# Optimization experiments

Measured on AMD Instinct MI355X. Metric: run time of the kernel, lower is better.

## Reference

```python
import jax, jax.numpy as jnp
import numpy as np
import math

B, H, L = 8, 512, 2048
CH = 1          # channels
D2 = 32         # d_state // 2 (conjugate pairs)
DT_MIN, DT_MAX = 0.001, 0.1


def setup_inputs() -> dict:
    key = jax.random.key(0)
    ks = jax.random.split(key, 7)
    u = jax.random.normal(ks[0], (B, H, L), dtype=jnp.float32)
    # Chebyshev initialization (SimpleS4)
    h_scale = jnp.exp(jnp.arange(H, dtype=jnp.float32) / H * math.log(DT_MAX / DT_MIN))
    angles = jnp.arange(D2, dtype=jnp.float32) * jnp.pi
    theta = jnp.broadcast_to(angles[None, None, :], (CH, H, D2)).astype(jnp.float32) + 0.0
    a = -(jnp.broadcast_to(h_scale[None, :, None], (CH, H, D2)).astype(jnp.float32) + 0.0)
    b = jax.random.normal(ks[1], (CH, H, D2), dtype=jnp.float32)
    c = jax.random.normal(ks[2], (CH, H, D2), dtype=jnp.float32)
    x0 = jax.random.normal(ks[3], (CH, H, D2), dtype=jnp.float32)
    D = jax.random.normal(ks[4], (CH, H), dtype=jnp.float32)
    lim = 1.0 / math.sqrt(CH * H)
    W = jax.random.uniform(ks[5], (H, CH * H), minval=-lim, maxval=lim, dtype=jnp.float32)
    bias = jax.random.uniform(ks[6], (H,), minval=-lim, maxval=lim, dtype=jnp.float32)
    return dict(u=u, a=a, theta=theta, b=b, c=c, x0=x0, D=D, W=W, bias=bias)


def fft_conv(u, f):
    # u: (B,H,L), f: (C,H,L) -> causal conv (B,C,H,L) via zero-padded FFT
    n = 2 * u.shape[-1]
    u_f = jnp.fft.rfft(u, n=n)
    f_f = jnp.fft.rfft(f, n=n)
    y = jnp.fft.irfft(jnp.einsum('bhl,chl->bchl', u_f, f_f), n=n)
    return y[..., : u.shape[-1]]


def s4_forward(u, a, theta, b, c, x0, D, W, bias):
    Bsz, Hd, l = u.shape
    T = 1.0 / (l - 1)                                   # quadrature step
    z = T * jnp.arange(l, dtype=u.dtype)                # (L,)
    aa = -jnp.abs(a)                                    # (C,H,D2) stable decay
    # Vandermonde-like basis: exp(a z) cos(theta z), shape (C,H,D2,L)
    base = jnp.exp(aa[..., None] * z) * jnp.cos(theta[..., None] * z)
    q = b * c                                           # (C,H,D2)
    f = 2.0 * T * jnp.einsum('chd,chdl->chl', q, base)  # SSM kernel (C,H,L)
    y = fft_conv(u, f)                                  # (B,C,H,L)
    # trapezoid-rule endpoint correction
    y = y - 0.5 * (jnp.einsum('ch,bhl->bchl', f[:, :, 0], u)
                   + jnp.einsum('chl,bh->bchl', f, u[:, :, 0]))
    # initial-state contribution (x0 term)
    k0 = 2.0 * jnp.einsum('chd,chdl->chl', c * x0, base)
    y = y + k0[None]
    # skip connection D*u
    y = y + jnp.einsum('ch,bhl->bchl', D, u)
    y = y.reshape(Bsz, CH * Hd, l)                      # (B, C*H, L)
    # NonLinear head: GELU -> pointwise Linear(C*H -> H) (transposed conv1x1)
    y = jax.nn.gelu(y, approximate=False)
    out = jnp.einsum('hf,bfl->bhl', W, y) + bias[None, :, None]
    return out


def reference(u, a, theta, b, c, x0, D, W, bias):
    return s4_forward(u, a, theta, b, c, x0, D, W, bias)
```

## Files before the change

### kernel.cpp

```cpp
#include <hip/hip_runtime.h>
#include <hip/hip_bf16.h>

#define B_  8
#define H_  512
#define L_  2048
#define D2_ 32
#define NC_ 64
#define LC_ 32
#define EP  36

typedef __attribute__((ext_vector_type(8))) short short8;
typedef __attribute__((ext_vector_type(8))) _Float16 half8;
typedef __attribute__((ext_vector_type(2))) _Float16 half2v;
typedef __attribute__((ext_vector_type(4))) float float4v;

__device__ __forceinline__ half2v pk_fma16(half2v a, half2v b, half2v c) {
    return __builtin_elementwise_fma(a, b, c);
}

__device__ __forceinline__ float gelu_fast(float x) {
    float q = x * fmaf(0.044715f, x * x, 1.0f);
    float s = __expf(-1.5957691216057308f * q);
    return __fdividef(x, 1.0f + s);
}

__device__ __forceinline__ unsigned pack_bf16x2(float x, float y) {
    __hip_bfloat162 p = __float22bfloat162_rn(make_float2(x, y));
    return *(unsigned*)&p;
}
__device__ __forceinline__ float2 unpack_bf16x2(unsigned v) {
    __hip_bfloat162 p = *(__hip_bfloat162*)&v;
    return __bfloat1622float2(p);
}
__device__ __forceinline__ unsigned pack_f16x2(float x, float y) {
    auto v = __builtin_amdgcn_cvt_pkrtz(x, y);
    return *(unsigned*)&v;
}

__device__ __forceinline__ void load_lds16(const void* g, void* l) {
    __builtin_amdgcn_global_load_lds((const __attribute__((address_space(1))) unsigned int*)g,
                                     (__attribute__((address_space(3))) unsigned int*)l, 16, 0, 0);
}

__global__ __launch_bounds__(256) void fkprep_kernel(
        const float* __restrict__ a, const float* __restrict__ th,
        const float* __restrict__ bb, const float* __restrict__ cc,
        const float* __restrict__ x0, const float* __restrict__ W,
        __hip_bfloat16* __restrict__ Wb, unsigned* __restrict__ FKf,
        _Float16* __restrict__ AB, _Float16* __restrict__ CB,
        _Float16* __restrict__ WPh) {
    __shared__ float avs[32], tvs[32], qds[32], gxs[32], f_lds[32];
    int h = blockIdx.x;
    int t = threadIdx.x;
    const float T = 1.0f / (float)(L_ - 1);
    Wb[(size_t)h * 512 + t]       = __float2bfloat16(W[(size_t)h * 512 + t]);
    Wb[(size_t)h * 512 + t + 256] = __float2bfloat16(W[(size_t)h * 512 + t + 256]);
    if (t < 32) {
        int d = t;
        float av = -fabsf(a[h * D2_ + d]);
        float tv = th[h * D2_ + d];
        avs[d] = av; tvs[d] = tv;
        qds[d] = bb[h * D2_ + d] * cc[h * D2_ + d];
        gxs[d] = 2.0f * cc[h * D2_ + d] * x0[h * D2_ + d];
        #pragma unroll
        for (int k = 0; k < 6; ++k) {
            float len = (float)(32 << k);
            float e2  = __expf(av * T * len);
            float an  = tv * T * len;
            WPh[((size_t)h * 6 + k) * 64 + d]      = (_Float16)(e2 * __cosf(an));
            WPh[((size_t)h * 6 + k) * 64 + 32 + d] = (_Float16)(e2 * __sinf(an));
        }
    }
    __syncthreads();
    int q4 = t & 3, lc = t >> 2;
    float z0 = T * (float)(lc * 32);
    float pr[8], pi[8], wr[8], wi[8], qd[8], gx[8];
    #pragma unroll
    for (int j = 0; j < 8; ++j) {
        int d = q4 * 8 + j;
        float aa = avs[d], tv = tvs[d];
        float e0 = __expf(aa * z0);
        pr[j] = e0 * __cosf(tv * z0);
        pi[j] = e0 * __sinf(tv * z0);
        float e1 = __expf(aa * T);
        wr[j] = e1 * __cosf(tv * T);
        wi[j] = e1 * __sinf(tv * T);
        qd[j] = qds[d];
        gx[j] = gxs[d];
    }
    for (int i = 0; i < 32; ++i) {
        float fa = 0.f, ka = 0.f;
        #pragma unroll
        for (int j = 0; j < 8; ++j) {
            fa = fmaf(qd[j], pr[j], fa);
            ka = fmaf(gx[j], pr[j], ka);
            float nr = fmaf(pr[j], wr[j], -(pi[j] * wi[j]));
            float ni = fmaf(pr[j], wi[j],  (pi[j] * wr[j]));
            pr[j] = nr; pi[j] = ni;
        }
        fa += __shfl_xor(fa, 1); fa += __shfl_xor(fa, 2);
        ka += __shfl_xor(ka, 1); ka += __shfl_xor(ka, 2);
        if (q4 == 0) {
            float fv = 2.0f * T * fa;
            FKf[(size_t)h * L_ + lc * 32 + i] = pack_bf16x2(fv, ka);
            if (lc == 0) f_lds[i] = fv;
        }
    }
    __syncthreads();
    for (int e = t; e < 64 * 32; e += 256) {
        int m = e >> 5, i = e & 31;
        int d = m & 31;
        float av = avs[d], tv = tvs[d];
        float z  = T * (float)(31 - i);
        float ex = __expf(av * z);
        float v  = (m < 32) ? ex * __cosf(tv * z) : ex * __sinf(tv * z);
        AB[(size_t)h * 2048 + e] = (_Float16)v;
    }
    for (int e = t; e < 32 * 96; e += 256) {
        int i = e / 96, k = e - i * 96;
        float v = 0.f;
        if (k < 32) {
            if (k <= i) v = f_lds[i - k];
        } else {
            int d = (k < 64) ? k - 32 : k - 64;
            float av = avs[d], tv = tvs[d];
            float qs = 2.0f * T * qds[d];
            float z  = T * (float)(i + 1);
            float ex = __expf(av * z);
            v = (k < 64) ? qs * ex * __cosf(tv * z) : -qs * ex * __sinf(tv * z);
        }
        CB[(size_t)h * 3072 + e] = (_Float16)v;
    }
}

__global__ __launch_bounds__(128, 6) void scan_mfma_kernel(
        const float* __restrict__ u, const _Float16* __restrict__ AB,
        const _Float16* __restrict__ CB, const unsigned* __restrict__ WPh,
        const float* __restrict__ Dp, const unsigned* __restrict__ FKf,
        __hip_bfloat16* __restrict__ y) {
    __shared__ __align__(16) unsigned El[64 * EP];
    int wid = threadIdx.x >> 6, lane = threadIdx.x & 63;
    int h = blockIdx.x, b = blockIdx.y;
    int ln = lane & 15, qq = lane >> 4;
    const float* ug = u + (size_t)(b * H_ + h) * L_;

    half8 uf[4];
    #pragma unroll
    for (int nb = 0; nb < 4; ++nb) {
        const float* p = ug + (nb * 16 + ln) * 32 + qq * 8;
        float4 a0 = *(const float4*)p;
        float4 a1 = *(const float4*)(p + 4);
        unsigned* vp = (unsigned*)&uf[nb];
        vp[0] = pack_f16x2(a0.x, a0.y);
        vp[1] = pack_f16x2(a0.z, a0.w);
        vp[2] = pack_f16x2(a1.x, a1.y);
        vp[3] = pack_f16x2(a1.z, a1.w);
    }

    const _Float16* ABh = AB + (size_t)h * 2048;
    int j0 = wid * 8 + qq * 2;
    #pragma unroll
    for (int e = 0; e < 2; ++e) {
        half8 af = *(const half8*)&ABh[(e * 32 + wid * 16 + ln) * 32 + qq * 8];
        #pragma unroll
        for (int nb = 0; nb < 4; ++nb) {
            float4v acc = (float4v){0.f, 0.f, 0.f, 0.f};
            acc = __builtin_amdgcn_mfma_f32_16x16x32_f16(af, uf[nb], acc, 0, 0, 0);
            unsigned p0 = pack_f16x2(acc[0], acc[1]);
            unsigned p1 = pack_f16x2(acc[2], acc[3]);
            *(uint2*)&El[(nb * 16 + ln) * EP + e * 16 + j0] = make_uint2(p0, p1);
        }
    }
    asm volatile("s_waitcnt lgkmcnt(0)" ::: "memory");
    __builtin_amdgcn_sched_barrier(0);

    int c = lane;
    unsigned sr[8], si[8];
    {
        const unsigned* rp = &El[c * EP + wid * 8];
        uint4 r0 = *(const uint4*)rp;
        uint4 r1 = *(const uint4*)(rp + 4);
        uint4 i0 = *(const uint4*)(rp + 16);
        uint4 i1 = *(const uint4*)(rp + 20);
        sr[0]=r0.x; sr[1]=r0.y; sr[2]=r0.z; sr[3]=r0.w;
        sr[4]=r1.x; sr[5]=r1.y; sr[6]=r1.z; sr[7]=r1.w;
        si[0]=i0.x; si[1]=i0.y; si[2]=i0.z; si[3]=i0.w;
        si[4]=i1.x; si[5]=i1.y; si[6]=i1.z; si[7]=i1.w;
    }
    const unsigned* mpb = WPh + (size_t)h * 6 * 32;
    #pragma unroll
    for (int st = 0; st < 6; ++st) {
        int off = 1 << st;
        int src = (c - off) & 63;
        bool act = c >= off;
        const unsigned* mp = mpb + st * 32 + wid * 8;
        #pragma unroll
        for (int jj = 0; jj < 8; ++jj) {
            unsigned prp = (unsigned)__shfl((int)sr[jj], src);
            unsigned pip = (unsigned)__shfl((int)si[jj], src);
            if (!act) { prp = 0u; pip = 0u; }
            unsigned mru = mp[jj];
            unsigned miu = mp[16 + jj];
            unsigned min_ = miu ^ 0x80008000u;
            half2v pr = *(half2v*)&prp, pi = *(half2v*)&pip;
            half2v Mr = *(half2v*)&mru, Mi = *(half2v*)&miu, Mni = *(half2v*)&min_;
            half2v s_r = *(half2v*)&sr[jj], s_i = *(half2v*)&si[jj];
            half2v nr = pk_fma16(pr, Mr, pk_fma16(pi, Mni, s_r));
            half2v ni = pk_fma16(pr, Mi, pk_fma16(pi, Mr,  s_i));
            sr[jj] = *(unsigned*)&nr; si[jj] = *(unsigned*)&ni;
        }
    }
    {
        int srcm1 = (c - 1) & 63;
        #pragma unroll
        for (int jj = 0; jj < 8; ++jj) {
            unsigned a0 = (unsigned)__shfl((int)sr[jj], srcm1);
            unsigned b0 = (unsigned)__shfl((int)si[jj], srcm1);
            if (c == 0) { a0 = 0u; b0 = 0u; }
            sr[jj] = a0; si[jj] = b0;
        }
    }
    {
        unsigned* wp = &El[c * EP + wid * 8];
        *(uint4*)wp        = make_uint4(sr[0], sr[1], sr[2], sr[3]);
        *(uint4*)(wp + 4)  = make_uint4(sr[4], sr[5], sr[6], sr[7]);
        *(uint4*)(wp + 16) = make_uint4(si[0], si[1], si[2], si[3]);
        *(uint4*)(wp + 20) = make_uint4(si[4], si[5], si[6], si[7]);
    }
    const unsigned* fgh = FKf + (size_t)h * L_;
    uint4 fkp[2][2];
    #pragma unroll
    for (int nbi = 0; nbi < 2; ++nbi) {
        int col = (2 * wid + nbi) * 16 + ln;
        fkp[nbi][0] = *(const uint4*)&fgh[col * 32 + qq * 4];
        fkp[nbi][1] = *(const uint4*)&fgh[col * 32 + 16 + qq * 4];
    }
    __syncthreads();

    const _Float16* CBh = CB + (size_t)h * 3072;
    float4v acc2[2][2];
    #pragma unroll
    for (int mb = 0; mb < 2; ++mb)
        #pragma unroll
        for (int nbi = 0; nbi < 2; ++nbi)
            acc2[mb][nbi] = (float4v){0.f, 0.f, 0.f, 0.f};
    #pragma unroll
    for (int ks = 0; ks < 3; ++ks) {
        half8 a2[2];
        a2[0] = *(const half8*)&CBh[(ln)      * 96 + ks * 32 + qq * 8];
        a2[1] = *(const half8*)&CBh[(16 + ln) * 96 + ks * 32 + qq * 8];
        #pragma unroll
        for (int nbi = 0; nbi < 2; ++nbi) {
            int col = (2 * wid + nbi) * 16 + ln;
            half8 bfv;
            if (ks == 0) bfv = uf[2 * wid + nbi];
            else {
                int off = (ks == 1) ? 0 : 16;
                bfv = *(const half8*)&El[col * EP + off + qq * 4];
            }
            acc2[0][nbi] = __builtin_amdgcn_mfma_f32_16x16x32_f16(a2[0], bfv, acc2[0][nbi], 0, 0, 0);
            acc2[1][nbi] = __builtin_amdgcn_mfma_f32_16x16x32_f16(a2[1], bfv, acc2[1][nbi], 0, 0, 0);
        }
    }

    float f0; { f0 = unpack_bf16x2(fgh[0]).x; }
    float c0v = Dp[h] - 0.5f * f0;
    float c1v = -0.5f * ug[0];
    #pragma unroll
    for (int nbi = 0; nbi < 2; ++nbi) {
        int col = (2 * wid + nbi) * 16 + ln;
        #pragma unroll
        for (int mb = 0; mb < 2; ++mb) {
            int l0 = col * 32 + mb * 16 + qq * 4;
            float4 u4 = *(const float4*)(ug + l0);
            uint4 fkv = fkp[nbi][mb];
            float us[4] = {u4.x, u4.y, u4.z, u4.w};
            unsigned fs[4] = {fkv.x, fkv.y, fkv.z, fkv.w};
            float g[4];
            #pragma unroll
            for (int r = 0; r < 4; ++r) {
                float2 fk = unpack_bf16x2(fs[r]);
                float yv = acc2[mb][nbi][r] + fmaf(c0v, us[r], fmaf(c1v, fk.x, fk.y));
                g[r] = gelu_fast(yv);
            }
            uint2 yo;
            yo.x = pack_bf16x2(g[0], g[1]);
            yo.y = pack_bf16x2(g[2], g[3]);
            *(uint2*)((short*)y + (size_t)(b * H_ + h) * L_ + l0) = yo;
        }
    }
}

__global__ __launch_bounds__(256) void gemm_kernel(
        const __hip_bfloat16* __restrict__ Wb, const __hip_bfloat16* __restrict__ y,
        const float* __restrict__ bias, float* __restrict__ out) {
    __shared__ __align__(16) short    As[64 * 32];
    __shared__ __align__(16) unsigned Bs[128 * 16];
    int h0 = blockIdx.x * 64;
    int l0 = blockIdx.y * 128;
    int b  = blockIdx.z;
    int t    = threadIdx.x;
    int lane = t & 63, wave = t >> 6;
    int m_off = (wave >> 1) * 32, n_off = (wave & 1) * 64;
    int quad = lane >> 4, ln = lane & 15;

    float4v acc[2][4];
    #pragma unroll
    for (int mt = 0; mt < 2; ++mt)
        #pragma unroll
        for (int nt = 0; nt < 4; ++nt)
            acc[mt][nt] = (float4v){0.f, 0.f, 0.f, 0.f};

    const short* Wg = (const short*)Wb;
    const short* Yg = (const short*)y + (size_t)b * 512 * L_;

    int r  = t >> 2;
    int qd = t & 3;
    int fp = t & 15;
    int n8 = t >> 4;

    for (int kt = 0; kt < 16; ++kt) {
        int k0 = kt * 32;
        load_lds16(Wg + (h0 + r) * 512 + k0 + qd * 8, &As[t * 8]);
        const short* ypa = Yg + (size_t)(k0 + 2 * fp) * L_ + l0 + n8 * 8;
        uint4 ya = *(const uint4*)ypa;
        uint4 yb = *(const uint4*)(ypa + L_);
        unsigned au[4] = {ya.x, ya.y, ya.z, ya.w};
        unsigned bu[4] = {yb.x, yb.y, yb.z, yb.w};
        unsigned pa[8];
        #pragma unroll
        for (int i2 = 0; i2 < 4; ++i2) {
            pa[2 * i2]     = (au[i2] & 0xFFFFu) | (bu[i2] << 16);
            pa[2 * i2 + 1] = (au[i2] >> 16)     | (bu[i2] & 0xFFFF0000u);
        }
        #pragma unroll
        for (int i = 0; i < 8; ++i) {
            int n = n8 * 8 + i;
            Bs[n * 16 + (fp ^ (((n >> 2) & 3) << 2))] = pa[i];
        }
        __syncthreads();

        short8 af[2], bf[4];
        #pragma unroll
        for (int mt = 0; mt < 2; ++mt)
            af[mt] = *(const short8*)&As[(m_off + mt * 16 + ln) * 32 + quad * 8];
        #pragma unroll
        for (int nt = 0; nt < 4; ++nt) {
            int n = n_off + nt * 16 + ln;
            bf[nt] = *(const short8*)&Bs[n * 16 + ((quad * 4) ^ (((n >> 2) & 3) << 2))];
        }
        #pragma unroll
        for (int mt = 0; mt < 2; ++mt)
            #pragma unroll
            for (int nt = 0; nt < 4; ++nt)
                acc[mt][nt] = __builtin_amdgcn_mfma_f32_16x16x32_bf16(
                    af[mt], bf[nt], acc[mt][nt], 0, 0, 0);
        __syncthreads();
    }

    #pragma unroll
    for (int mt = 0; mt < 2; ++mt) {
        #pragma unroll
        for (int nt = 0; nt < 4; ++nt) {
            int hh = h0 + m_off + mt * 16 + quad * 4;
            int ll = l0 + n_off + nt * 16 + ln;
            #pragma unroll
            for (int r2 = 0; r2 < 4; ++r2)
                out[((size_t)(b * H_ + hh + r2)) * L_ + ll] = acc[mt][nt][r2] + bias[hh + r2];
        }
    }
}

extern "C" void kernel_launch(void* const* d_in, const int* in_sizes, int n_in,
                              void* d_out, int out_size, void* d_ws, size_t ws_size,
                              hipStream_t stream) {
    const float* u    = (const float*)d_in[0];
    const float* a    = (const float*)d_in[1];
    const float* th   = (const float*)d_in[2];
    const float* bb   = (const float*)d_in[3];
    const float* cc   = (const float*)d_in[4];
    const float* x0   = (const float*)d_in[5];
    const float* Dp   = (const float*)d_in[6];
    const float* W    = (const float*)d_in[7];
    const float* bias = (const float*)d_in[8];
    float* out = (float*)d_out;
    char* ws = (char*)d_ws;

    unsigned*       FKf = (unsigned*)ws;
    __hip_bfloat16* y   = (__hip_bfloat16*)(ws + (20ull << 20));
    __hip_bfloat16* Wb  = (__hip_bfloat16*)(ws + (36ull << 20));
    _Float16*       AB  = (_Float16*)(ws + (37ull << 20));
    _Float16*       CB  = (_Float16*)(ws + (39ull << 20));
    _Float16*       WPh = (_Float16*)(ws + (42ull << 20));

    hipLaunchKernelGGL(fkprep_kernel,     dim3(H_),        dim3(256), 0, stream,
                       a, th, bb, cc, x0, W, Wb, FKf, AB, CB, WPh);
    hipLaunchKernelGGL(scan_mfma_kernel,  dim3(H_, B_),    dim3(128), 0, stream,
                       u, AB, CB, (const unsigned*)WPh, Dp, FKf, y);
    hipLaunchKernelGGL(gemm_kernel,       dim3(8, 16, 8),  dim3(256), 0, stream,
                       Wb, y, bias, out);
}
```

Before: 165.7 us.

## Double-buffer GEMM LDS tiles and coalesce FK kernel stores via shared memory

The GEMM kernel now uses two LDS buffers and prefetches the next K-tile of W (async global-to-LDS) and y (into registers) while running MFMAs on the current tile. This removes one barrier per iteration and hides global load latency. The prep kernel now stages its packed FK values in shared memory and writes them out as contiguous 16-byte stores instead of strided scalar stores. The cost is twice the LDS in the GEMM and extra register pressure from the prefetched values.

After: 163.8 us. About the same (-1.2%).

```diff
diff --git a/kernel.cpp b/kernel.cpp
--- a/kernel.cpp
+++ b/kernel.cpp
@@ -50,6 +50,7 @@
         _Float16* __restrict__ AB, _Float16* __restrict__ CB,
         _Float16* __restrict__ WPh) {
     __shared__ float avs[32], tvs[32], qds[32], gxs[32], f_lds[32];
+    __shared__ unsigned fk_all[32 * 64];
     int h = blockIdx.x;
     int t = threadIdx.x;
     const float T = 1.0f / (float)(L_ - 1);
@@ -102,11 +103,22 @@
         ka += __shfl_xor(ka, 1); ka += __shfl_xor(ka, 2);
         if (q4 == 0) {
             float fv = 2.0f * T * fa;
-            FKf[(size_t)h * L_ + lc * 32 + i] = pack_bf16x2(fv, ka);
+            fk_all[i * 64 + lc] = pack_bf16x2(fv, ka);
             if (lc == 0) f_lds[i] = fv;
         }
     }
     __syncthreads();
+    {
+        unsigned v[8];
+        #pragma unroll
+        for (int j = 0; j < 8; ++j) {
+            int l = t * 8 + j;
+            v[j] = fk_all[(l & 31) * 64 + (l >> 5)];
+        }
+        uint4* dst = (uint4*)(FKf + (size_t)h * L_ + t * 8);
+        dst[0] = make_uint4(v[0], v[1], v[2], v[3]);
+        dst[1] = make_uint4(v[4], v[5], v[6], v[7]);
+    }
     for (int e = t; e < 64 * 32; e += 256) {
         int m = e >> 5, i = e & 31;
         int d = m & 31;
@@ -294,8 +306,8 @@
 __global__ __launch_bounds__(256) void gemm_kernel(
         const __hip_bfloat16* __restrict__ Wb, const __hip_bfloat16* __restrict__ y,
         const float* __restrict__ bias, float* __restrict__ out) {
-    __shared__ __align__(16) short    As[64 * 32];
-    __shared__ __align__(16) unsigned Bs[128 * 16];
+    __shared__ __align__(16) short    As[2][64 * 32];
+    __shared__ __align__(16) unsigned Bs[2][128 * 16];
     int h0 = blockIdx.x * 64;
     int l0 = blockIdx.y * 128;
     int b  = blockIdx.z;
@@ -318,36 +330,38 @@
     int qd = t & 3;
     int fp = t & 15;
     int n8 = t >> 4;
-
-    for (int kt = 0; kt < 16; ++kt) {
-        int k0 = kt * 32;
-        load_lds16(Wg + (h0 + r) * 512 + k0 + qd * 8, &As[t * 8]);
-        const short* ypa = Yg + (size_t)(k0 + 2 * fp) * L_ + l0 + n8 * 8;
-        uint4 ya = *(const uint4*)ypa;
-        uint4 yb = *(const uint4*)(ypa + L_);
+    const short* ybase = Yg + (size_t)(2 * fp) * L_ + l0 + n8 * 8;
+
+    load_lds16(Wg + (h0 + r) * 512 + qd * 8, &As[0][t * 8]);
+    {
+        uint4 ya = *(const uint4*)ybase;
+        uint4 yb = *(const uint4*)(ybase + L_);
         unsigned au[4] = {ya.x, ya.y, ya.z, ya.w};
         unsigned bu[4] = {yb.x, yb.y, yb.z, yb.w};
-        unsigned pa[8];
         #pragma unroll
         for (int i2 = 0; i2 < 4; ++i2) {
-            pa[2 * i2]     = (au[i2] & 0xFFFFu) | (bu[i2] << 16);
-            pa[2 * i2 + 1] = (au[i2] >> 16)     | (bu[i2] & 0xFFFF0000u);
-        }
-        #pragma unroll
-        for (int i = 0; i < 8; ++i) {
-            int n = n8 * 8 + i;
-            Bs[n * 16 + (fp ^ (((n >> 2) & 3) << 2))] = pa[i];
-        }
-        __syncthreads();
+            int na = n8 * 8 + 2 * i2, nb = na + 1;
+            Bs[0][na * 16 + (fp ^ (((na >> 2) & 3) << 2))] = (au[i2] & 0xFFFFu) | (bu[i2] << 16);
+            Bs[0][nb * 16 + (fp ^ (((nb >> 2) & 3) << 2))] = (au[i2] >> 16) | (bu[i2] & 0xFFFF0000u);
+        }
+    }
+    __syncthreads();
+
+    for (int kt = 0; kt < 15; ++kt) {
+        int cur = kt & 1, nxt = cur ^ 1;
+        int k1 = (kt + 1) * 32;
+        load_lds16(Wg + (h0 + r) * 512 + k1 + qd * 8, &As[nxt][t * 8]);
+        uint4 za = *(const uint4*)(ybase + (size_t)k1 * L_);
+        uint4 zb = *(const uint4*)(ybase + (size_t)(k1 + 1) * L_);
 
         short8 af[2], bf[4];
         #pragma unroll
         for (int mt = 0; mt < 2; ++mt)
-            af[mt] = *(const short8*)&As[(m_off + mt * 16 + ln) * 32 + quad * 8];
+            af[mt] = *(const short8*)&As[cur][(m_off + mt * 16 + ln) * 32 + quad * 8];
         #pragma unroll
         for (int nt = 0; nt < 4; ++nt) {
             int n = n_off + nt * 16 + ln;
-            bf[nt] = *(const short8*)&Bs[n * 16 + ((quad * 4) ^ (((n >> 2) & 3) << 2))];
+            bf[nt] = *(const short8*)&Bs[cur][n * 16 + ((quad * 4) ^ (((n >> 2) & 3) << 2))];
         }
         #pragma unroll
         for (int mt = 0; mt < 2; ++mt)
@@ -355,7 +369,36 @@
             for (int nt = 0; nt < 4; ++nt)
                 acc[mt][nt] = __builtin_amdgcn_mfma_f32_16x16x32_bf16(
                     af[mt], bf[nt], acc[mt][nt], 0, 0, 0);
+        __builtin_amdgcn_sched_barrier(0);
+
+        {
+            unsigned au[4] = {za.x, za.y, za.z, za.w};
+            unsigned bu[4] = {zb.x, zb.y, zb.z, zb.w};
+            #pragma unroll
+            for (int i2 = 0; i2 < 4; ++i2) {
+                int na = n8 * 8 + 2 * i2, nb = na + 1;
+                Bs[nxt][na * 16 + (fp ^ (((na >> 2) & 3) << 2))] = (au[i2] & 0xFFFFu) | (bu[i2] << 16);
+                Bs[nxt][nb * 16 + (fp ^ (((nb >> 2) & 3) << 2))] = (au[i2] >> 16) | (bu[i2] & 0xFFFF0000u);
+            }
+        }
         __syncthreads();
+    }
+    {
+        short8 af[2], bf[4];
+        #pragma unroll
+        for (int mt = 0; mt < 2; ++mt)
+            af[mt] = *(const short8*)&As[1][(m_off + mt * 16 + ln) * 32 + quad * 8];
+        #pragma unroll
+        for (int nt = 0; nt < 4; ++nt) {
+            int n = n_off + nt * 16 + ln;
+            bf[nt] = *(const short8*)&Bs[1][n * 16 + ((quad * 4) ^ (((n >> 2) & 3) << 2))];
+        }
+        #pragma unroll
+        for (int mt = 0; mt < 2; ++mt)
+            #pragma unroll
+            for (int nt = 0; nt < 4; ++nt)
+                acc[mt][nt] = __builtin_amdgcn_mfma_f32_16x16x32_bf16(
+                    af[mt], bf[nt], acc[mt][nt], 0, 0, 0);
     }
 
     #pragma unroll
```
